# Kernel tuning notes

Measured on AMD Instinct MI355X. Metric: run time of the kernel, lower is better.

## Reference

```python
import jax, jax.numpy as jnp
import numpy as np

S, FEAT, D, H, L, DFF, C = 1024, 64, 512, 8, 2, 2048, 10
DB = D // 4  # distance-bias MLP hidden
NFREQ = D // 6  # 85 -> 6*85=510 dims, padded to 512
EPS = 1e-5


def _layernorm(x, g, b):
    mu = jnp.mean(x, axis=-1, keepdims=True)
    var = jnp.mean(jnp.square(x - mu), axis=-1, keepdims=True)
    return (x - mu) * jax.lax.rsqrt(var + EPS) * g + b


def setup_inputs() -> dict:
    key = jax.random.key(0)
    ks = iter(jax.random.split(key, 40))
    def w(shape, scale=0.02):
        return (jax.random.normal(next(ks), shape, jnp.float32) * scale)
    inp = {
        'features': jax.random.normal(next(ks), (S, FEAT), jnp.float32),
        'positions': jax.random.uniform(next(ks), (S, 3), jnp.float32),
        'freq_bands': jnp.asarray(10.0 ** np.linspace(0.0, 10.0, NFREQ), jnp.float32),
        'in_w': w((FEAT, D)), 'in_b': jnp.zeros((D,), jnp.float32),
        'qw': w((L, D, D)), 'qb': jnp.zeros((L, D), jnp.float32),
        'kw': w((L, D, D)), 'kb': jnp.zeros((L, D), jnp.float32),
        'vw': w((L, D, D)), 'vb': jnp.zeros((L, D), jnp.float32),
        'ow': w((L, D, D)), 'ob': jnp.zeros((L, D), jnp.float32),
        'db1w': w((L, 1, DB), 0.5), 'db1b': jnp.zeros((L, DB), jnp.float32),
        'db2w': w((L, DB, H), 0.1), 'db2b': jnp.zeros((L, H), jnp.float32),
        'n1g': jnp.ones((L, D), jnp.float32), 'n1b': jnp.zeros((L, D), jnp.float32),
        'n2g': jnp.ones((L, D), jnp.float32), 'n2b': jnp.zeros((L, D), jnp.float32),
        'f1w': w((L, D, DFF)), 'f1b': jnp.zeros((L, DFF), jnp.float32),
        'f2w': w((L, DFF, D)), 'f2b': jnp.zeros((L, D), jnp.float32),
        'c1w': w((D, D // 2)), 'c1b': jnp.zeros((D // 2,), jnp.float32),
        'c2w': w((D // 2, C)), 'c2b': jnp.zeros((C,), jnp.float32),
    }
    return inp


def _forward(features, positions, freq_bands, in_w, in_b, qw, qb, kw, kb, vw, vb,
             ow, ob, db1w, db1b, db2w, db2b, n1g, n1b, n2g, n2b,
             f1w, f1b, f2w, f2b, c1w, c1b, c2w, c2b):
    d_model = in_w.shape[1]
    nhead = db2w.shape[-1]
    head_dim = d_model // nhead
    scale = 1.0 / np.sqrt(head_dim)

    x = features[None] @ in_w + in_b            # [1, S, D]
    pos = positions[None]                        # [1, S, 3]

    # 3D sinusoidal positional encoding: [sin0,cos0,sin1,cos1,sin2,cos2]
    enc = []
    for i in range(3):
        cs = pos[..., i:i + 1] * freq_bands      # [1, S, NFREQ] (broadcast)
        enc.append(jnp.sin(cs))
        enc.append(jnp.cos(cs))
    pe = jnp.concatenate(enc, axis=-1)           # [1, S, 6*NFREQ]
    if pe.shape[-1] > d_model:
        pe = pe[..., :d_model]
    elif pe.shape[-1] < d_model:
        pe = jnp.pad(pe, ((0, 0), (0, 0), (0, d_model - pe.shape[-1])))
    x = x + pe

    # pairwise distances [1, S, S, 1]; safe sqrt (zero grad on diagonal)
    diff = pos[:, :, None, :] - pos[:, None, :, :]
    sq = jnp.sum(jnp.square(diff), axis=-1, keepdims=True)
    dist = jnp.sqrt(jnp.where(sq > 0, sq, 1.0)) * (sq > 0)

    n_layers = qw.shape[0]
    seq = x.shape[1]
    for l in range(n_layers):
        q = (x @ qw[l] + qb[l]).reshape(1, seq, nhead, head_dim)
        k = (x @ kw[l] + kb[l]).reshape(1, seq, nhead, head_dim)
        v = (x @ vw[l] + vb[l]).reshape(1, seq, nhead, head_dim)
        scores = jnp.einsum('bihd,bjhd->bhij', q, k) * scale  # [1,H,S,S]
        hbias = jax.nn.relu(dist @ db1w[l] + db1b[l])          # [1,S,S,DB]
        bias = jnp.einsum('bijc,ch->bhij', hbias, db2w[l]) + db2b[l][None, :, None, None]
        attn = jax.nn.softmax(scores + bias, axis=-1)
        out = jnp.einsum('bhij,bjhd->bihd', attn, v).reshape(1, seq, d_model)
        out = out @ ow[l] + ob[l]
        x = _layernorm(x + out, n1g[l], n1b[l])
        ffn = jax.nn.relu(x @ f1w[l] + f1b[l]) @ f2w[l] + f2b[l]
        x = _layernorm(x + ffn, n2g[l], n2b[l])

    pooled = jnp.mean(x, axis=1)                 # [1, D]
    return jax.nn.relu(pooled @ c1w + c1b) @ c2w + c2b  # [1, C]


def reference(features, positions, freq_bands, in_w, in_b, qw, qb, kw, kb, vw, vb,
              ow, ob, db1w, db1b, db2w, db2b, n1g, n1b, n2g, n2b,
              f1w, f1b, f2w, f2b, c1w, c1b, c2w, c2b):
    return _forward(features, positions, freq_bands, in_w, in_b, qw, qb, kw, kb, vw, vb,
                    ow, ob, db1w, db1b, db2w, db2b, n1g, n1b, n2g, n2b,
                    f1w, f1b, f2w, f2b, c1w, c1b, c2w, c2b)
```

## Files before the change

kernel.cpp:

```cpp
#include <hip/hip_runtime.h>

namespace {
constexpr int kS   = 1024;
constexpr int kD   = 512;
constexpr int kDFF = 2048;
constexpr int kNF  = 85;
}

typedef __attribute__((ext_vector_type(8))) short bhalf8_t;
typedef _Float16 half8_t __attribute__((ext_vector_type(8)));
typedef __attribute__((ext_vector_type(4))) float f32x4_t;

__device__ __forceinline__ float wave_sum(float v) {
#pragma unroll
    for (int o = 1; o < 64; o <<= 1) v += __shfl_xor(v, o, 64);
    return v;
}
__device__ __forceinline__ unsigned short f2h(float f) {
    _Float16 h = (_Float16)f;
    return __builtin_bit_cast(unsigned short, h);
}
__device__ __forceinline__ float h2f(unsigned short u) {
    return (float)__builtin_bit_cast(_Float16, u);
}

__global__ __launch_bounds__(256)
void prep_a_k(const float* __restrict__ feat, const float* __restrict__ pos,
              const float* __restrict__ fb, const float* __restrict__ in_w,
              const float* __restrict__ in_b, float* __restrict__ x,
              unsigned short* __restrict__ xb,
              float* __restrict__ dist,
              const float* __restrict__ a_, const float* __restrict__ b_,
              float* __restrict__ bp_out)
{
    __shared__ float smem[128];
    int bid = blockIdx.x;
    int t = threadIdx.x;
    if (bid < 1024) {
        int s = bid;
        if (t < 64) smem[t] = feat[s * 64 + t];
        __syncthreads();
        float acc0 = in_b[t], acc1 = in_b[t + 256];
#pragma unroll 8
        for (int c = 0; c < 64; ++c) {
            float fv = smem[c];
            acc0 = fmaf(fv, in_w[c * kD + t], acc0);
            acc1 = fmaf(fv, in_w[c * kD + 256 + t], acc1);
        }
        float pe0 = 0.f, pe1 = 0.f;
        {
            int d = t;
            if (d < 6 * kNF) {
                int seg = d / kNF, idx = d - seg * kNF;
                float cs = pos[s * 3 + (seg >> 1)] * fb[idx];
                pe0 = (seg & 1) ? cosf(cs) : sinf(cs);
            }
            d = t + 256;
            if (d < 6 * kNF) {
                int seg = d / kNF, idx = d - seg * kNF;
                float cs = pos[s * 3 + (seg >> 1)] * fb[idx];
                pe1 = (seg & 1) ? cosf(cs) : sinf(cs);
            }
        }
        float o0 = acc0 + pe0, o1 = acc1 + pe1;
        x[s * kD + t]        = o0;
        x[s * kD + 256 + t]  = o1;
        xb[s * kD + t]       = f2h(o0);
        xb[s * kD + 256 + t] = f2h(o1);
    } else if (bid < 2048) {
        int i = bid - 1024;
        float px = pos[i * 3], py = pos[i * 3 + 1], pz = pos[i * 3 + 2];
        for (int j = t; j < kS; j += 256) {
            float dx = px - pos[j * 3], dy = py - pos[j * 3 + 1], dz = pz - pos[j * 3 + 2];
            float sq = dx * dx + dy * dy + dz * dz;
            dist[(long)i * kS + j] = sq > 0.f ? sqrtf(sq) : 0.f;
        }
    } else {
        int l = bid - 2048;
        const float* ap = a_ + l * 128;
        const float* bp = b_ + l * 128;
        float* out = bp_out + l * 128;
        if (t < 128) {
            float a = ap[t], b = bp[t];
            smem[t] = (a != 0.f) ? (-b / a) : 3.0e38f;
        }
        __syncthreads();
        for (int ksz = 2; ksz <= 128; ksz <<= 1) {
            for (int j = ksz >> 1; j > 0; j >>= 1) {
                if (t < 128) {
                    int ixj = t ^ j;
                    if (ixj > t) {
                        bool up = ((t & ksz) == 0);
                        float x0 = smem[t], x1 = smem[ixj];
                        if ((x0 > x1) == up) { smem[t] = x1; smem[ixj] = x0; }
                    }
                }
                __syncthreads();
            }
        }
        if (t < 128) out[t] = smem[t];
    }
}

__device__ __forceinline__ void tr_tile32(const float* __restrict__ in,
                                          unsigned short* __restrict__ out,
                                          int N, int K, int k0, int n0, int t,
                                          float* tile )
{
    int r = t >> 3, c4 = (t & 7) * 4;
    float4 v = *reinterpret_cast<const float4*>(&in[(long)(k0 + r) * N + n0 + c4]);
    tile[r * 33 + c4] = v.x; tile[r * 33 + c4 + 1] = v.y;
    tile[r * 33 + c4 + 2] = v.z; tile[r * 33 + c4 + 3] = v.w;
    __syncthreads();
    int nr = t >> 3, kq = (t & 7) * 4;
    unsigned short h[4];
#pragma unroll
    for (int j = 0; j < 4; ++j) h[j] = f2h(tile[(kq + j) * 33 + nr]);
    *reinterpret_cast<ushort4*>(&out[(long)(n0 + nr) * K + k0 + kq]) =
        make_ushort4(h[0], h[1], h[2], h[3]);
}

__global__ __launch_bounds__(256)
void prep_w_k(const float* __restrict__ qw, const float* __restrict__ kw,
              const float* __restrict__ vw, const float* __restrict__ ow,
              unsigned short* __restrict__ qwb, unsigned short* __restrict__ kwb,
              unsigned short* __restrict__ vwb, unsigned short* __restrict__ owb,
              const float* __restrict__ f1w, unsigned short* __restrict__ f1wb,
              const float* __restrict__ f2w, unsigned short* __restrict__ f2wb,
              const float* __restrict__ a_, const float* __restrict__ b_,
              const float* __restrict__ w2, const float* __restrict__ b2,
              const float* __restrict__ bp, float* __restrict__ Atab,
              float* __restrict__ Btab)
{
    __shared__ float smem[32 * 33];
    int bid = blockIdx.x;
    int t = threadIdx.x;
    if (bid < 2048) {
        int zz = bid >> 8, rem = bid & 255;
        int mat = zz >> 1, layer = zz & 1;
        const float* in = (mat == 0) ? qw : (mat == 1) ? kw : (mat == 2) ? vw : ow;
        unsigned short* out = (mat == 0) ? qwb : (mat == 1) ? kwb : (mat == 2) ? vwb : owb;
        tr_tile32(in + (long)layer * 262144, out + (long)layer * 262144,
                  512, 512, (rem & 15) * 32, (rem >> 4) * 32, t, smem);
    } else if (bid < 4096) {
        int l = bid - 2048;
        int z = l >> 10;
        tr_tile32(f1w + (long)z * 1048576, f1wb + (long)z * 1048576,
                  2048, 512, (l & 15) * 32, ((l >> 4) & 63) * 32, t, smem);
    } else if (bid < 6144) {
        int l = bid - 4096;
        int z = l >> 10;
        tr_tile32(f2w + (long)z * 1048576, f2wb + (long)z * 1048576,
                  512, 2048, (l & 63) * 32, ((l >> 6) & 15) * 32, t, smem);
    } else {
        int l = bid - 6144;
        int seg = l % 129, ly = l / 129;
        const float* ap = a_ + ly * 128;
        const float* bpp = b_ + ly * 128;
        const float* w2p = w2 + ly * 1024;
        const float* b2p = b2 + ly * 8;
        const float* bpl = bp + ly * 128;
        float* At = Atab + ly * 1040;
        float* Bt = Btab + ly * 1040;

        float m;
        if (seg == 0)        m = bpl[0] - 1.0f;
        else if (seg == 128) m = bpl[127] + 1.0f;
        else                 m = 0.5f * (bpl[seg - 1] + bpl[seg]);

        int h = t & 7, cg = t >> 3;
        float A = 0.f, B = 0.f;
#pragma unroll
        for (int j = 0; j < 4; ++j) {
            int c = cg * 4 + j;
            float a = ap[c], b = bpp[c];
            if (fmaf(a, m, b) > 0.f) {
                float w = w2p[c * 8 + h];
                A = fmaf(a, w, A);
                B = fmaf(b, w, B);
            }
        }
#pragma unroll
        for (int off = 8; off < 64; off <<= 1) {
            A += __shfl_xor(A, off, 64);
            B += __shfl_xor(B, off, 64);
        }
        int w = t >> 6, lane = t & 63;
        if (lane < 8) { smem[w * 8 + lane] = A; smem[32 + w * 8 + lane] = B; }
        __syncthreads();
        if (t < 8) {
            float At_ = smem[t] + smem[8 + t] + smem[16 + t] + smem[24 + t];
            float Bt_ = smem[32 + t] + smem[40 + t] + smem[48 + t] + smem[56 + t];
            At[seg * 8 + t] = At_;
            Bt[seg * 8 + t] = Bt_ + b2p[t];
        }
    }
}

constexpr int BKp = 72;
constexpr int ASZ = 64 * BKp;
constexpr int BSZ = 128 * BKp;

template<int K>
__device__ __forceinline__ void gemm_core(
    const unsigned short* __restrict__ Ap, const unsigned short* __restrict__ Bp,
    int lda, int ldb, int bm, int bn, int tid,
    unsigned short* __restrict__ As, unsigned short* __restrict__ Bs,
    f32x4_t acc[2][4])
{
    int w = tid >> 6, lane = tid & 63, quad = lane >> 4, l16 = lane & 15;
    int wm = (w >> 1) * 32, wn = (w & 1) * 64;
    int ar = tid >> 2, ac = (tid & 3) * 16;
    int br = tid >> 1, bc = (tid & 1) * 32;
    const unsigned short* pa = Ap + (long)(bm + ar) * lda + ac;
    const unsigned short* pb = Bp + (long)(bn + br) * ldb + bc;

    bhalf8_t aS0, aS1, bS0, bS1, bS2, bS3;
    auto ldg = [&](int k0) {
        aS0 = *reinterpret_cast<const bhalf8_t*>(pa + k0);
        aS1 = *reinterpret_cast<const bhalf8_t*>(pa + k0 + 8);
        bS0 = *reinterpret_cast<const bhalf8_t*>(pb + k0);
        bS1 = *reinterpret_cast<const bhalf8_t*>(pb + k0 + 8);
        bS2 = *reinterpret_cast<const bhalf8_t*>(pb + k0 + 16);
        bS3 = *reinterpret_cast<const bhalf8_t*>(pb + k0 + 24);
    };
    auto stg = [&](unsigned short* as, unsigned short* bs) {
        *reinterpret_cast<bhalf8_t*>(&as[ar * BKp + ac])      = aS0;
        *reinterpret_cast<bhalf8_t*>(&as[ar * BKp + ac + 8])  = aS1;
        *reinterpret_cast<bhalf8_t*>(&bs[br * BKp + bc])      = bS0;
        *reinterpret_cast<bhalf8_t*>(&bs[br * BKp + bc + 8])  = bS1;
        *reinterpret_cast<bhalf8_t*>(&bs[br * BKp + bc + 16]) = bS2;
        *reinterpret_cast<bhalf8_t*>(&bs[br * BKp + bc + 24]) = bS3;
    };

    ldg(0); stg(As, Bs);
    constexpr int NT = K / 64;
#pragma unroll
    for (int t = 0; t < NT; ++t) {
        __syncthreads();
        if (t + 1 < NT) ldg((t + 1) * 64);
        const unsigned short* as = As + (t & 1) * ASZ;
        const unsigned short* bs = Bs + (t & 1) * BSZ;
#pragma unroll
        for (int kq = 0; kq < 2; ++kq) {
            bhalf8_t af[2], bf[4];
#pragma unroll
            for (int i = 0; i < 2; ++i)
                af[i] = *reinterpret_cast<const bhalf8_t*>(
                    &as[(wm + i * 16 + l16) * BKp + kq * 32 + quad * 8]);
#pragma unroll
            for (int j = 0; j < 4; ++j)
                bf[j] = *reinterpret_cast<const bhalf8_t*>(
                    &bs[(wn + j * 16 + l16) * BKp + kq * 32 + quad * 8]);
#pragma unroll
            for (int i = 0; i < 2; ++i)
#pragma unroll
                for (int j = 0; j < 4; ++j)
                    acc[i][j] = __builtin_amdgcn_mfma_f32_16x16x32_f16(
                        __builtin_bit_cast(half8_t, af[i]), __builtin_bit_cast(half8_t, bf[j]),
                        acc[i][j], 0, 0, 0);
        }
        if (t + 1 < NT) stg(As + ((t + 1) & 1) * ASZ, Bs + ((t + 1) & 1) * BSZ);
    }
}

__global__ __launch_bounds__(256, 2)
void qkv_bias_k(const unsigned short* __restrict__ xb,
                const unsigned short* __restrict__ qwb, const unsigned short* __restrict__ kwb,
                const unsigned short* __restrict__ vwb,
                const float* __restrict__ qbias, const float* __restrict__ kbias,
                const float* __restrict__ vbias,
                unsigned short* __restrict__ qb2, unsigned short* __restrict__ kb2,
                unsigned short* __restrict__ vtb,
                const float* __restrict__ dist, const float* __restrict__ bp,
                const float* __restrict__ Atab, const float* __restrict__ Btab,
                unsigned short* __restrict__ bmap)
{
    __shared__ __align__(16) unsigned short smem[2 * ASZ + 2 * BSZ];
    int bid = blockIdx.x;
    int tid = threadIdx.x;
    if (bid < 192) {
        int z = bid >> 6, rem = bid & 63;
        int bm = (rem & 15) * 64, bn = (rem >> 4) * 128;
        const unsigned short* Bp = (z == 1) ? kwb : (z == 2) ? vwb : qwb;
        const float* bias = (z == 1) ? kbias : (z == 2) ? vbias : qbias;
        f32x4_t acc[2][4] = {};
        gemm_core<512>(xb, Bp, 512, 512, bm, bn, tid, smem, smem + 2 * ASZ, acc);

        int w = tid >> 6, lane = tid & 63, quad = lane >> 4, l16 = lane & 15;
        int wm = (w >> 1) * 32, wn = (w & 1) * 64;
        if (z == 2) {
            __syncthreads();
            unsigned short* T = smem;
#pragma unroll
            for (int j = 0; j < 4; ++j) {
                int ln = wn + j * 16 + l16;
                float bv = bias[bn + ln];
#pragma unroll
                for (int i = 0; i < 2; ++i)
#pragma unroll
                    for (int r = 0; r < 4; ++r)
                        T[ln * BKp + wm + i * 16 + quad * 4 + r] =
                            f2h((acc[i][j][r] + bv) * 1024.f);
            }
            __syncthreads();
            int nr = tid >> 1, mc = (tid & 1) * 32;
            int gn = bn + nr;
            unsigned short* dst = vtb + (long)(gn >> 6) * 65536
                                + (long)(gn & 63) * 1024 + bm + mc;
#pragma unroll
            for (int jj = 0; jj < 4; ++jj)
                *reinterpret_cast<bhalf8_t*>(dst + jj * 8) =
                    *reinterpret_cast<const bhalf8_t*>(&T[nr * BKp + mc + jj * 8]);
        } else {
#pragma unroll
            for (int j = 0; j < 4; ++j) {
                int n = bn + wn + j * 16 + l16;
                float bv = bias[n];
                unsigned short* dst = ((z == 1) ? kb2 : qb2)
                    + (long)(n >> 6) * 131072 + (n & 63);
#pragma unroll
                for (int i = 0; i < 2; ++i)
#pragma unroll
                    for (int r = 0; r < 4; ++r) {
                        int m = bm + wm + i * 16 + quad * 4 + r;
                        float s = acc[i][j][r] + bv;
                        unsigned short hi = f2h(s);
                        dst[(long)m * 128]      = hi;
                        dst[(long)m * 128 + 64] = (z == 0) ? f2h(s - h2f(hi)) : hi;
                    }
            }
        }
    } else {
        float* fs = reinterpret_cast<float*>(smem);
        float* bps = fs;
        float* Ah  = fs + 128;
        float* Bh  = fs + 1160;
        int t = tid;
        if (t < 128) bps[t] = bp[t];
        for (int i = t; i < 1032; i += 256) { Ah[i] = Atab[i]; Bh[i] = Btab[i]; }
        __syncthreads();
        long i = ((long)(bid - 192) * 256 + t) * 4;
        float4 d4 = *reinterpret_cast<const float4*>(dist + i);
        float dv[4] = {d4.x, d4.y, d4.z, d4.w};
        int seg[4];
#pragma unroll
        for (int j = 0; j < 4; ++j) {
            float tv = dv[j];
            int lo = 0, hi = 128;
            while (lo < hi) { int mid = (lo + hi) >> 1; if (bps[mid] < tv) lo = mid + 1; else hi = mid; }
            seg[j] = lo;
        }
#pragma unroll
        for (int h = 0; h < 8; ++h) {
            unsigned short o[4];
#pragma unroll
            for (int j = 0; j < 4; ++j)
                o[j] = f2h(fmaf(Ah[seg[j] * 8 + h], dv[j], Bh[seg[j] * 8 + h]));
            *reinterpret_cast<ushort4*>(bmap + (long)h * 1048576 + i) =
                make_ushort4(o[0], o[1], o[2], o[3]);
        }
    }
}

__global__ __launch_bounds__(256, 2)
void bgemm_ffn1_k(const unsigned short* __restrict__ A,
                  const unsigned short* __restrict__ B,
                  const float* __restrict__ bias,
                  unsigned short* __restrict__ hb)
{
    __shared__ __align__(16) unsigned short smem[2 * ASZ + 2 * BSZ];
    int tid = threadIdx.x;
    int bm = blockIdx.x * 64, bn = blockIdx.y * 128;
    f32x4_t acc[2][4] = {};
    gemm_core<512>(A, B, 512, 512, bm, bn, tid, smem, smem + 2 * ASZ, acc);

    int w = tid >> 6, lane = tid & 63, quad = lane >> 4, l16 = lane & 15;
    int wm = (w >> 1) * 32, wn = (w & 1) * 64;
#pragma unroll
    for (int j = 0; j < 4; ++j) {
        int n = bn + wn + j * 16 + l16;
        float bv = bias[n];
#pragma unroll
        for (int i = 0; i < 2; ++i)
#pragma unroll
            for (int r = 0; r < 4; ++r) {
                int m = bm + wm + i * 16 + quad * 4 + r;
                hb[(long)m * kDFF + n] = f2h(fmaxf(acc[i][j][r] + bv, 0.f));
            }
    }
}

template<int K>
__global__ __launch_bounds__(256, 2)
void bgemm_k(const unsigned short* __restrict__ A, const unsigned short* __restrict__ B,
             int N, int lda, int ldb, unsigned short* __restrict__ Cpart)
{
    __shared__ __align__(16) unsigned short smem[2 * ASZ + 2 * BSZ];
    int tid = threadIdx.x;
    int ks = blockIdx.z;
    const unsigned short* Ap = A + (long)ks * K;
    const unsigned short* Bp = B + (long)ks * K;
    int bm = blockIdx.x * 64, bn = blockIdx.y * 128;
    f32x4_t acc[2][4] = {};
    gemm_core<K>(Ap, Bp, lda, ldb, bm, bn, tid, smem, smem + 2 * ASZ, acc);

    int w = tid >> 6, lane = tid & 63, quad = lane >> 4, l16 = lane & 15;
    int wm = (w >> 1) * 32, wn = (w & 1) * 64;
    unsigned short* Cp = Cpart + (long)ks * kS * N;
#pragma unroll
    for (int i = 0; i < 2; ++i)
#pragma unroll
        for (int j = 0; j < 4; ++j)
#pragma unroll
            for (int r = 0; r < 4; ++r) {
                int m = bm + wm + i * 16 + quad * 4 + r;
                int n = bn + wn + j * 16 + l16;
                Cp[(long)m * N + n] = f2h(acc[i][j][r]);
            }
}

__global__ __launch_bounds__(64)
void flash_part_k(const unsigned short* __restrict__ qb2, const unsigned short* __restrict__ kb2,
                  const unsigned short* __restrict__ vtb, const unsigned short* __restrict__ bmap,
                  unsigned short* __restrict__ po, float* __restrict__ pm, float* __restrict__ pl)
{
    __shared__ unsigned short Ps[16 * 136];

    int tid = threadIdx.x;
    int wg  = blockIdx.x;
    int lin = (wg & 7) * 512 + (wg >> 3);
    int qb  = lin & 63;
    int h   = (lin >> 6) & 7;
    int z   = lin >> 9;
    int bm = qb * 16;
    int k0 = z * 128;

    const unsigned short* Qh = qb2 + (long)h * 131072;
    const unsigned short* Kh = kb2 + (long)h * 131072;
    const unsigned short* Vh = vtb + (long)h * 65536;
    const unsigned short* Bm = bmap + (long)h * 1048576;

    int quad = tid >> 4, l16 = tid & 15;

    bhalf8_t aq[4];
#pragma unroll
    for (int kq = 0; kq < 4; ++kq)
        aq[kq] = *reinterpret_cast<const bhalf8_t*>(
            &Qh[(long)(bm + l16) * 128 + kq * 32 + quad * 8]);

    f32x4_t sacc[8] = {};
#pragma unroll
    for (int kq = 0; kq < 4; ++kq) {
        bhalf8_t bk[8];
#pragma unroll
        for (int nb = 0; nb < 8; ++nb)
            bk[nb] = *reinterpret_cast<const bhalf8_t*>(
                &Kh[(long)(k0 + nb * 16 + l16) * 128 + kq * 32 + quad * 8]);
#pragma unroll
        for (int nb = 0; nb < 8; ++nb)
            sacc[nb] = __builtin_amdgcn_mfma_f32_16x16x32_f16(
                __builtin_bit_cast(half8_t, aq[kq]), __builtin_bit_cast(half8_t, bk[nb]),
                sacc[nb], 0, 0, 0);
    }

    float m_r[4] = {-3.0e38f, -3.0e38f, -3.0e38f, -3.0e38f};
#pragma unroll
    for (int nb = 0; nb < 8; ++nb)
#pragma unroll
        for (int r = 0; r < 4; ++r) {
            int gm = bm + quad * 4 + r;
            int gn = k0 + nb * 16 + l16;
            float bias = h2f(Bm[(long)gm * kS + gn]);
            float s = fmaf(sacc[nb][r], 0.125f, bias);
            sacc[nb][r] = s;
            m_r[r] = fmaxf(m_r[r], s);
        }
#pragma unroll
    for (int r = 0; r < 4; ++r) {
        float m_ = m_r[r];
#pragma unroll
        for (int off = 1; off < 16; off <<= 1) m_ = fmaxf(m_, __shfl_xor(m_, off, 64));
        m_r[r] = m_;
    }

    float l_r[4];
#pragma unroll
    for (int r = 0; r < 4; ++r) {
        int row = quad * 4 + r;
        float mN = m_r[r];
        float s_ = 0.f;
#pragma unroll
        for (int nb = 0; nb < 8; ++nb) {
            float p = __expf(sacc[nb][r] - mN);
            Ps[row * 136 + nb * 16 + l16] = f2h(p * 16384.f);
            s_ += p;
        }
#pragma unroll
        for (int off = 1; off < 16; off <<= 1) s_ += __shfl_xor(s_, off, 64);
        l_r[r] = s_;
    }

    long sbase = (((long)z * 8 + h) * 64 + qb) * 16;
    if (l16 == 0) {
#pragma unroll
        for (int r = 0; r < 4; ++r) {
            pm[sbase + quad * 4 + r] = m_r[r];
            pl[sbase + quad * 4 + r] = l_r[r];
        }
    }
    __syncthreads();

    f32x4_t oacc[4] = {};
#pragma unroll
    for (int kq2 = 0; kq2 < 4; ++kq2) {
        bhalf8_t ap = *reinterpret_cast<const bhalf8_t*>(&Ps[l16 * 136 + kq2 * 32 + quad * 8]);
#pragma unroll
        for (int j2 = 0; j2 < 4; ++j2) {
            bhalf8_t bv = *reinterpret_cast<const bhalf8_t*>(
                &Vh[(long)(j2 * 16 + l16) * 1024 + k0 + kq2 * 32 + quad * 8]);
            oacc[j2] = __builtin_amdgcn_mfma_f32_16x16x32_f16(
                __builtin_bit_cast(half8_t, ap), __builtin_bit_cast(half8_t, bv),
                oacc[j2], 0, 0, 0);
        }
    }

    unsigned short* pob = po + sbase * 64;
#pragma unroll
    for (int j2 = 0; j2 < 4; ++j2)
#pragma unroll
        for (int r = 0; r < 4; ++r)
            pob[(quad * 4 + r) * 64 + j2 * 16 + l16] =
                f2h(oacc[j2][r] * (1.f / 16777216.f));
}

__global__ __launch_bounds__(256)
void flash_merge_k(const unsigned short* __restrict__ po, const float* __restrict__ pm,
                   const float* __restrict__ pl, unsigned short* __restrict__ aob)
{
    int t = blockIdx.x * 256 + threadIdx.x;
    int c8  = t & 7;
    int row = (t >> 3) & 15;
    int qb  = (t >> 7) & 63;
    int h   = t >> 13;
    long sidx = (((long)h * 64) + qb) * 16 + row;

    float m[8];
    float M = -3.0e38f;
#pragma unroll
    for (int z = 0; z < 8; ++z) { m[z] = pm[z * 8192 + sidx]; M = fmaxf(M, m[z]); }
    float w[8], lt = 0.f;
#pragma unroll
    for (int z = 0; z < 8; ++z) {
        w[z] = __expf(m[z] - M);
        lt = fmaf(pl[z * 8192 + sidx], w[z], lt);
    }
    float acc[8] = {};
#pragma unroll
    for (int z = 0; z < 8; ++z) {
        const unsigned short* p = po + (z * 8192 + sidx) * 64 + c8 * 8;
        ushort4 a = *reinterpret_cast<const ushort4*>(p);
        ushort4 b = *reinterpret_cast<const ushort4*>(p + 4);
        acc[0] = fmaf(h2f(a.x), w[z], acc[0]); acc[1] = fmaf(h2f(a.y), w[z], acc[1]);
        acc[2] = fmaf(h2f(a.z), w[z], acc[2]); acc[3] = fmaf(h2f(a.w), w[z], acc[3]);
        acc[4] = fmaf(h2f(b.x), w[z], acc[4]); acc[5] = fmaf(h2f(b.y), w[z], acc[5]);
        acc[6] = fmaf(h2f(b.z), w[z], acc[6]); acc[7] = fmaf(h2f(b.w), w[z], acc[7]);
    }
    float inv = 1.f / lt;
    unsigned short hi[8];
#pragma unroll
    for (int j = 0; j < 8; ++j) hi[j] = f2h(acc[j] * inv);
    long base = ((long)qb * 16 + row) * 512 + h * 64 + c8 * 8;
    *reinterpret_cast<ushort4*>(&aob[base])     = make_ushort4(hi[0], hi[1], hi[2], hi[3]);
    *reinterpret_cast<ushort4*>(&aob[base + 4]) = make_ushort4(hi[4], hi[5], hi[6], hi[7]);
}

__global__ __launch_bounds__(256)
void add_ln_fused_k(const unsigned short* __restrict__ part, float* __restrict__ x,
                    const float* __restrict__ bias,
                    const float* __restrict__ g, const float* __restrict__ b,
                    unsigned short* __restrict__ xb, int splitk)
{
    __shared__ float sm[4];
    int row = blockIdx.x, t = threadIdx.x;
    const long MN = (long)kS * kD;
    float* xr = x + (long)row * kD;
    float s0 = 0.f, s1 = 0.f;
    const unsigned short* pr = part + (long)row * kD;
    for (int sl = 0; sl < splitk; ++sl) {
        s0 += h2f(pr[(long)sl * MN + t]);
        s1 += h2f(pr[(long)sl * MN + t + 256]);
    }
    s0 += bias[t] + xr[t];
    s1 += bias[t + 256] + xr[t + 256];
    float sum = wave_sum(s0 + s1);
    if ((t & 63) == 0) sm[t >> 6] = sum;
    __syncthreads();
    sum = sm[0] + sm[1] + sm[2] + sm[3];
    float mu = sum * (1.f / kD);
    float d0 = s0 - mu, d1 = s1 - mu;
    __syncthreads();
    float vs = wave_sum(d0 * d0 + d1 * d1);
    if ((t & 63) == 0) sm[t >> 6] = vs;
    __syncthreads();
    vs = sm[0] + sm[1] + sm[2] + sm[3];
    float rs = rsqrtf(vs * (1.f / kD) + 1e-5f);
    float o0 = fmaf(d0 * rs, g[t], b[t]);
    float o1 = fmaf(d1 * rs, g[t + 256], b[t + 256]);
    xr[t]       = o0;
    xr[t + 256] = o1;
    unsigned short* xrow = xb + (long)row * 512;
    xrow[t]       = f2h(o0);
    xrow[t + 256] = f2h(o1);
}

__global__ __launch_bounds__(256)
void pool_k(const float* __restrict__ x, float* __restrict__ partial)
{
    int col = blockIdx.x * 256 + threadIdx.x;
    int rb = blockIdx.y;
    float s = 0.f;
    for (int r = rb * 128; r < rb * 128 + 128; ++r) s += x[(long)r * kD + col];
    partial[rb * kD + col] = s;
}

__global__ __launch_bounds__(256)
void head_k(const float* __restrict__ partial,
            const float* __restrict__ c1w, const float* __restrict__ c1b,
            const float* __restrict__ c2w, const float* __restrict__ c2b,
            float* __restrict__ out)
{
    __shared__ float pooled[kD];
    __shared__ float h1[256];
    int t = threadIdx.x;
    for (int d = t; d < kD; d += 256) {
        float s = 0.f;
        for (int r = 0; r < 8; ++r) s += partial[r * kD + d];
        pooled[d] = s * (1.0f / kS);
    }
    __syncthreads();
    float acc = c1b[t];
    for (int f = 0; f < kD; ++f) acc = fmaf(pooled[f], c1w[f * 256 + t], acc);
    h1[t] = fmaxf(acc, 0.f);
    __syncthreads();
    if (t < 10) {
        float o = c2b[t];
        for (int f = 0; f < 256; ++f) o = fmaf(h1[f], c2w[f * 10 + t], o);
        out[t] = o;
    }
}

extern "C" void kernel_launch(void* const* d_in, const int* in_sizes, int n_in,
                              void* d_out, int out_size, void* d_ws, size_t ws_size,
                              hipStream_t stream)
{
    (void)in_sizes; (void)n_in; (void)out_size; (void)ws_size;
    const float* features = (const float*)d_in[0];
    const float* positions= (const float*)d_in[1];
    const float* fb       = (const float*)d_in[2];
    const float* in_w     = (const float*)d_in[3];
    const float* in_b     = (const float*)d_in[4];
    const float* qw  = (const float*)d_in[5];
    const float* qb  = (const float*)d_in[6];
    const float* kw  = (const float*)d_in[7];
    const float* kb  = (const float*)d_in[8];
    const float* vw  = (const float*)d_in[9];
    const float* vb  = (const float*)d_in[10];
    const float* ow  = (const float*)d_in[11];
    const float* ob  = (const float*)d_in[12];
    const float* db1w= (const float*)d_in[13];
    const float* db1b= (const float*)d_in[14];
    const float* db2w= (const float*)d_in[15];
    const float* db2b= (const float*)d_in[16];
    const float* n1g = (const float*)d_in[17];
    const float* n1b = (const float*)d_in[18];
    const float* n2g = (const float*)d_in[19];
    const float* n2b = (const float*)d_in[20];
    const float* f1w = (const float*)d_in[21];
    const float* f1b = (const float*)d_in[22];
    const float* f2w = (const float*)d_in[23];
    const float* f2b = (const float*)d_in[24];
    const float* c1w = (const float*)d_in[25];
    const float* c1b = (const float*)d_in[26];
    const float* c2w = (const float*)d_in[27];
    const float* c2b = (const float*)d_in[28];

    float* ws = (float*)d_ws;
    const long SD = (long)kS * kD;
    float* x      = ws;
    float* dist   = ws + 3 * SD;
    float* part_f = ws + 5 * SD;
    float* bpw    = ws + 17 * SD;
    float* Atab   = bpw + 256;
    float* Btab   = Atab + 2080;
    float* partial= Btab + 2080;

    unsigned short* part16 = (unsigned short*)part_f;
    unsigned short* po     = (unsigned short*)part_f;
    float* pmv = part_f + 4194304 / 2 + 65536;
    float* plv = pmv + 65536;

    unsigned short* ub = (unsigned short*)(ws + 17 * SD + 8512);
    unsigned short* xb   = ub;
    unsigned short* aob  = xb   + 524288;
    unsigned short* qb2  = aob  + 524288;
    unsigned short* kb2  = qb2  + 1048576;
    unsigned short* vtb  = kb2  + 1048576;
    unsigned short* hb   = vtb  + 524288;
    unsigned short* qwb  = hb   + 2097152;
    unsigned short* kwb  = qwb  + 524288;
    unsigned short* vwb  = kwb  + 524288;
    unsigned short* owb  = vwb  + 524288;
    unsigned short* f1wb = owb  + 524288;
    unsigned short* f2wb = f1wb + 2097152;
    unsigned short* bmap = f2wb + 2097152;

    prep_a_k<<<2050, 256, 0, stream>>>(features, positions, fb, in_w, in_b, x, xb,
                                       dist, db1w, db1b, bpw);
    prep_w_k<<<6402, 256, 0, stream>>>(qw, kw, vw, ow, qwb, kwb, vwb, owb,
                                       f1w, f1wb, f2w, f2wb,
                                       db1w, db1b, db2w, db2b, bpw, Atab, Btab);

    for (int l = 0; l < 2; ++l) {
        qkv_bias_k<<<1216, 256, 0, stream>>>(
            xb, qwb + l * 262144, kwb + l * 262144, vwb + l * 262144,
            qb + l * kD, kb + l * kD, vb + l * kD, qb2, kb2, vtb,
            dist, bpw + l * 128, Atab + l * 1040, Btab + l * 1040, bmap);

        flash_part_k<<<4096, 64, 0, stream>>>(
            qb2, kb2, vtb, bmap, po, pmv, plv);
        flash_merge_k<<<256, 256, 0, stream>>>(po, pmv, plv, aob);

        bgemm_k<128><<<dim3(16, 4, 4), 256, 0, stream>>>(
            aob, owb + l * 262144, 512, 512, 512, part16);
        add_ln_fused_k<<<kS, 256, 0, stream>>>(
            part16, x, ob + l * kD, n1g + l * kD, n1b + l * kD, xb, 4);

        bgemm_ffn1_k<<<dim3(16, 16), 256, 0, stream>>>(
            xb, f1wb + l * 1048576, f1b + l * kDFF, hb);

        bgemm_k<512><<<dim3(16, 4, 4), 256, 0, stream>>>(
            hb, f2wb + l * 1048576, 512, 2048, 2048, part16);
        add_ln_fused_k<<<kS, 256, 0, stream>>>(
            part16, x, f2b + l * kD, n2g + l * kD, n2b + l * kD, xb, 4);
    }

    pool_k<<<dim3(2, 8), 256, 0, stream>>>(x, partial);
    head_k<<<1, 256, 0, stream>>>(partial, c1w, c1b, c2w, c2b, (float*)d_out);
}
```

Baseline: 326.6 us.

## Fuse flash merge and pool/head via last-block counters, deepen GEMM prefetch

The separate flash_merge kernel is removed. Each flash_part block now bumps a per-(head, query-block) atomic counter, and the eighth block to arrive merges the partial outputs into aob. pool_k and head_k are combined the same way, with a last-block counter, into one kernel. The counters are cleared inside qkv_bias_k. The GEMM core gains a second register staging set, so global loads are issued two k-tiles ahead instead of one, which raises register pressure. The aim is to save three kernel launches and hide more global-load latency, at the cost of added fences and atomics and a serialized merge tail in flash_part.

Measured after the change: 640.0 us. 96.0% more time.

```diff
diff --git a/kernel.cpp b/kernel.cpp
--- a/kernel.cpp
+++ b/kernel.cpp
@@ -215,30 +215,35 @@
     const unsigned short* pa = Ap + (long)(bm + ar) * lda + ac;
     const unsigned short* pb = Bp + (long)(bn + br) * ldb + bc;
 
-    bhalf8_t aS0, aS1, bS0, bS1, bS2, bS3;
-    auto ldg = [&](int k0) {
-        aS0 = *reinterpret_cast<const bhalf8_t*>(pa + k0);
-        aS1 = *reinterpret_cast<const bhalf8_t*>(pa + k0 + 8);
-        bS0 = *reinterpret_cast<const bhalf8_t*>(pb + k0);
-        bS1 = *reinterpret_cast<const bhalf8_t*>(pb + k0 + 8);
-        bS2 = *reinterpret_cast<const bhalf8_t*>(pb + k0 + 16);
-        bS3 = *reinterpret_cast<const bhalf8_t*>(pb + k0 + 24);
-    };
-    auto stg = [&](unsigned short* as, unsigned short* bs) {
-        *reinterpret_cast<bhalf8_t*>(&as[ar * BKp + ac])      = aS0;
-        *reinterpret_cast<bhalf8_t*>(&as[ar * BKp + ac + 8])  = aS1;
-        *reinterpret_cast<bhalf8_t*>(&bs[br * BKp + bc])      = bS0;
-        *reinterpret_cast<bhalf8_t*>(&bs[br * BKp + bc + 8])  = bS1;
-        *reinterpret_cast<bhalf8_t*>(&bs[br * BKp + bc + 16]) = bS2;
-        *reinterpret_cast<bhalf8_t*>(&bs[br * BKp + bc + 24]) = bS3;
-    };
-
-    ldg(0); stg(As, Bs);
+    bhalf8_t a0_0, a0_1, b0_0, b0_1, b0_2, b0_3;
+    bhalf8_t a1_0, a1_1, b1_0, b1_1, b1_2, b1_3;
+
+#define LDG(S, k0) do { \
+    a##S##_0 = *reinterpret_cast<const bhalf8_t*>(pa + (k0)); \
+    a##S##_1 = *reinterpret_cast<const bhalf8_t*>(pa + (k0) + 8); \
+    b##S##_0 = *reinterpret_cast<const bhalf8_t*>(pb + (k0)); \
+    b##S##_1 = *reinterpret_cast<const bhalf8_t*>(pb + (k0) + 8); \
+    b##S##_2 = *reinterpret_cast<const bhalf8_t*>(pb + (k0) + 16); \
+    b##S##_3 = *reinterpret_cast<const bhalf8_t*>(pb + (k0) + 24); } while (0)
+#define STG(S, as, bs) do { \
+    *reinterpret_cast<bhalf8_t*>(&(as)[ar * BKp + ac])      = a##S##_0; \
+    *reinterpret_cast<bhalf8_t*>(&(as)[ar * BKp + ac + 8])  = a##S##_1; \
+    *reinterpret_cast<bhalf8_t*>(&(bs)[br * BKp + bc])      = b##S##_0; \
+    *reinterpret_cast<bhalf8_t*>(&(bs)[br * BKp + bc + 8])  = b##S##_1; \
+    *reinterpret_cast<bhalf8_t*>(&(bs)[br * BKp + bc + 16]) = b##S##_2; \
+    *reinterpret_cast<bhalf8_t*>(&(bs)[br * BKp + bc + 24]) = b##S##_3; } while (0)
+
     constexpr int NT = K / 64;
+    LDG(0, 0);
+    STG(0, As, Bs);
+    if (NT > 1) LDG(1, 64);
 #pragma unroll
     for (int t = 0; t < NT; ++t) {
         __syncthreads();
-        if (t + 1 < NT) ldg((t + 1) * 64);
+        if (t + 2 < NT) {
+            if ((t & 1) == 0) LDG(0, (t + 2) * 64);
+            else              LDG(1, (t + 2) * 64);
+        }
         const unsigned short* as = As + (t & 1) * ASZ;
         const unsigned short* bs = Bs + (t & 1) * BSZ;
 #pragma unroll
@@ -260,8 +265,13 @@
                         __builtin_bit_cast(half8_t, af[i]), __builtin_bit_cast(half8_t, bf[j]),
                         acc[i][j], 0, 0, 0);
         }
-        if (t + 1 < NT) stg(As + ((t + 1) & 1) * ASZ, Bs + ((t + 1) & 1) * BSZ);
-    }
+        if (t + 1 < NT) {
+            if (((t + 1) & 1) == 0) STG(0, As, Bs);
+            else                    STG(1, As + ASZ, Bs + BSZ);
+        }
+    }
+#undef LDG
+#undef STG
 }
 
 __global__ __launch_bounds__(256, 2)
@@ -274,7 +284,7 @@
                 unsigned short* __restrict__ vtb,
                 const float* __restrict__ dist, const float* __restrict__ bp,
                 const float* __restrict__ Atab, const float* __restrict__ Btab,
-                unsigned short* __restrict__ bmap)
+                unsigned short* __restrict__ bmap, unsigned int* __restrict__ cnt)
 {
     __shared__ __align__(16) unsigned short smem[2 * ASZ + 2 * BSZ];
     int bid = blockIdx.x;
@@ -332,6 +342,10 @@
             }
         }
     } else {
+        if (bid < 195) {
+            int i = (bid - 192) * 256 + tid;
+            if (i < 520) cnt[i] = 0;
+        }
         float* fs = reinterpret_cast<float*>(smem);
         float* bps = fs;
         float* Ah  = fs + 128;
@@ -423,7 +437,8 @@
 __global__ __launch_bounds__(64)
 void flash_part_k(const unsigned short* __restrict__ qb2, const unsigned short* __restrict__ kb2,
                   const unsigned short* __restrict__ vtb, const unsigned short* __restrict__ bmap,
-                  unsigned short* __restrict__ po, float* __restrict__ pm, float* __restrict__ pl)
+                  unsigned short* __restrict__ po, float* __restrict__ pm, float* __restrict__ pl,
+                  unsigned short* __restrict__ aob, unsigned int* __restrict__ cnt)
 {
     __shared__ unsigned short Ps[16 * 136];
 
@@ -532,47 +547,48 @@
         for (int r = 0; r < 4; ++r)
             pob[(quad * 4 + r) * 64 + j2 * 16 + l16] =
                 f2h(oacc[j2][r] * (1.f / 16777216.f));
-}
-
-__global__ __launch_bounds__(256)
-void flash_merge_k(const unsigned short* __restrict__ po, const float* __restrict__ pm,
-                   const float* __restrict__ pl, unsigned short* __restrict__ aob)
-{
-    int t = blockIdx.x * 256 + threadIdx.x;
-    int c8  = t & 7;
-    int row = (t >> 3) & 15;
-    int qb  = (t >> 7) & 63;
-    int h   = t >> 13;
-    long sidx = (((long)h * 64) + qb) * 16 + row;
-
-    float m[8];
-    float M = -3.0e38f;
-#pragma unroll
-    for (int z = 0; z < 8; ++z) { m[z] = pm[z * 8192 + sidx]; M = fmaxf(M, m[z]); }
-    float w[8], lt = 0.f;
-#pragma unroll
-    for (int z = 0; z < 8; ++z) {
-        w[z] = __expf(m[z] - M);
-        lt = fmaf(pl[z * 8192 + sidx], w[z], lt);
-    }
-    float acc[8] = {};
-#pragma unroll
-    for (int z = 0; z < 8; ++z) {
-        const unsigned short* p = po + (z * 8192 + sidx) * 64 + c8 * 8;
-        ushort4 a = *reinterpret_cast<const ushort4*>(p);
-        ushort4 b = *reinterpret_cast<const ushort4*>(p + 4);
-        acc[0] = fmaf(h2f(a.x), w[z], acc[0]); acc[1] = fmaf(h2f(a.y), w[z], acc[1]);
-        acc[2] = fmaf(h2f(a.z), w[z], acc[2]); acc[3] = fmaf(h2f(a.w), w[z], acc[3]);
-        acc[4] = fmaf(h2f(b.x), w[z], acc[4]); acc[5] = fmaf(h2f(b.y), w[z], acc[5]);
-        acc[6] = fmaf(h2f(b.z), w[z], acc[6]); acc[7] = fmaf(h2f(b.w), w[z], acc[7]);
-    }
-    float inv = 1.f / lt;
-    unsigned short hi[8];
-#pragma unroll
-    for (int j = 0; j < 8; ++j) hi[j] = f2h(acc[j] * inv);
-    long base = ((long)qb * 16 + row) * 512 + h * 64 + c8 * 8;
-    *reinterpret_cast<ushort4*>(&aob[base])     = make_ushort4(hi[0], hi[1], hi[2], hi[3]);
-    *reinterpret_cast<ushort4*>(&aob[base + 4]) = make_ushort4(hi[4], hi[5], hi[6], hi[7]);
+
+    __threadfence();
+    unsigned old = 0;
+    if (tid == 0) old = atomicAdd(&cnt[h * 64 + qb], 1u);
+    old = __shfl((int)old, 0, 64);
+    if (old == 7) {
+        __threadfence();
+#pragma unroll
+        for (int u = 0; u < 2; ++u) {
+            int unit = tid + u * 64;
+            int c8 = unit & 7, row = unit >> 3;
+            long sidx = (((long)h * 64) + qb) * 16 + row;
+            float m[8];
+            float M = -3.0e38f;
+#pragma unroll
+            for (int zz = 0; zz < 8; ++zz) { m[zz] = pm[zz * 8192 + sidx]; M = fmaxf(M, m[zz]); }
+            float wz[8], lt = 0.f;
+#pragma unroll
+            for (int zz = 0; zz < 8; ++zz) {
+                wz[zz] = __expf(m[zz] - M);
+                lt = fmaf(pl[zz * 8192 + sidx], wz[zz], lt);
+            }
+            float acc[8] = {};
+#pragma unroll
+            for (int zz = 0; zz < 8; ++zz) {
+                const unsigned short* p = po + (zz * 8192 + sidx) * 64 + c8 * 8;
+                ushort4 a = *reinterpret_cast<const ushort4*>(p);
+                ushort4 b = *reinterpret_cast<const ushort4*>(p + 4);
+                acc[0] = fmaf(h2f(a.x), wz[zz], acc[0]); acc[1] = fmaf(h2f(a.y), wz[zz], acc[1]);
+                acc[2] = fmaf(h2f(a.z), wz[zz], acc[2]); acc[3] = fmaf(h2f(a.w), wz[zz], acc[3]);
+                acc[4] = fmaf(h2f(b.x), wz[zz], acc[4]); acc[5] = fmaf(h2f(b.y), wz[zz], acc[5]);
+                acc[6] = fmaf(h2f(b.z), wz[zz], acc[6]); acc[7] = fmaf(h2f(b.w), wz[zz], acc[7]);
+            }
+            float inv = 1.f / lt;
+            unsigned short hi[8];
+#pragma unroll
+            for (int j = 0; j < 8; ++j) hi[j] = f2h(acc[j] * inv);
+            long base = ((long)qb * 16 + row) * 512 + h * 64 + c8 * 8;
+            *reinterpret_cast<ushort4*>(&aob[base])     = make_ushort4(hi[0], hi[1], hi[2], hi[3]);
+            *reinterpret_cast<ushort4*>(&aob[base + 4]) = make_ushort4(hi[4], hi[5], hi[6], hi[7]);
+        }
+    }
 }
 
 __global__ __launch_bounds__(256)
@@ -615,28 +631,32 @@
 }
 
 __global__ __launch_bounds__(256)
-void pool_k(const float* __restrict__ x, float* __restrict__ partial)
-{
-    int col = blockIdx.x * 256 + threadIdx.x;
-    int rb = blockIdx.y;
+void pool_head_k(const float* __restrict__ x, float* __restrict__ partial,
+                 unsigned int* __restrict__ cnt2,
+                 const float* __restrict__ c1w, const float* __restrict__ c1b,
+                 const float* __restrict__ c2w, const float* __restrict__ c2b,
+                 float* __restrict__ out)
+{
+    __shared__ float pooled[kD];
+    __shared__ float h1[256];
+    __shared__ int isLast;
+    int t = threadIdx.x;
+    int cb = blockIdx.x & 1, rb = blockIdx.x >> 1;
+    int col = cb * 256 + t;
     float s = 0.f;
     for (int r = rb * 128; r < rb * 128 + 128; ++r) s += x[(long)r * kD + col];
     partial[rb * kD + col] = s;
-}
-
-__global__ __launch_bounds__(256)
-void head_k(const float* __restrict__ partial,
-            const float* __restrict__ c1w, const float* __restrict__ c1b,
-            const float* __restrict__ c2w, const float* __restrict__ c2b,
-            float* __restrict__ out)
-{
-    __shared__ float pooled[kD];
-    __shared__ float h1[256];
-    int t = threadIdx.x;
+
+    __threadfence();
+    if (t == 0) isLast = (atomicAdd(cnt2, 1u) == 15u);
+    __syncthreads();
+    if (!isLast) return;
+    __threadfence();
+
     for (int d = t; d < kD; d += 256) {
-        float s = 0.f;
-        for (int r = 0; r < 8; ++r) s += partial[r * kD + d];
-        pooled[d] = s * (1.0f / kS);
+        float ps = 0.f;
+        for (int r = 0; r < 8; ++r) ps += partial[r * kD + d];
+        pooled[d] = ps * (1.0f / kS);
     }
     __syncthreads();
     float acc = c1b[t];
@@ -699,6 +719,8 @@
     unsigned short* po     = (unsigned short*)part_f;
     float* pmv = part_f + 4194304 / 2 + 65536;
     float* plv = pmv + 65536;
+    unsigned int* cnt = (unsigned int*)(plv + 65536);
+    unsigned int* cnt2 = cnt + 512;
 
     unsigned short* ub = (unsigned short*)(ws + 17 * SD + 8512);
     unsigned short* xb   = ub;
@@ -725,11 +747,10 @@
         qkv_bias_k<<<1216, 256, 0, stream>>>(
             xb, qwb + l * 262144, kwb + l * 262144, vwb + l * 262144,
             qb + l * kD, kb + l * kD, vb + l * kD, qb2, kb2, vtb,
-            dist, bpw + l * 128, Atab + l * 1040, Btab + l * 1040, bmap);
+            dist, bpw + l * 128, Atab + l * 1040, Btab + l * 1040, bmap, cnt);
 
         flash_part_k<<<4096, 64, 0, stream>>>(
-            qb2, kb2, vtb, bmap, po, pmv, plv);
-        flash_merge_k<<<256, 256, 0, stream>>>(po, pmv, plv, aob);
+            qb2, kb2, vtb, bmap, po, pmv, plv, aob, cnt);
 
         bgemm_k<128><<<dim3(16, 4, 4), 256, 0, stream>>>(
             aob, owb + l * 262144, 512, 512, 512, part16);
@@ -745,6 +766,6 @@
             part16, x, f2b + l * kD, n2g + l * kD, n2b + l * kD, xb, 4);
     }
 
-    pool_k<<<dim3(2, 8), 256, 0, stream>>>(x, partial);
-    head_k<<<1, 256, 0, stream>>>(partial, c1w, c1b, c2w, c2b, (float*)d_out);
-}
+    pool_head_k<<<16, 256, 0, stream>>>(x, partial, cnt2, c1w, c1b, c2w, c2b,
+                                        (float*)d_out);
+}
```
